# Performance work log

Measured on AMD Instinct MI355X. Metric: run time of the kernel, lower is better.

## Reference

```python
import jax, jax.numpy as jnp
import numpy as np

N_HEAD = 16


def setup_inputs() -> dict:
    key = jax.random.key(0)
    k1, k2, k3 = jax.random.split(key, 3)
    B, T, C = 4, 2048, 1024
    x = jax.random.normal(k1, (B, T, C), dtype=jnp.float32)
    W = jax.random.normal(k2, (3 * C, C), dtype=jnp.float32) * (1.0 / np.sqrt(C))
    b = jax.random.normal(k3, (3 * C,), dtype=jnp.float32) * 0.02
    return {"x": x, "W": W, "b": b, "input_pos": 0}


def reference(x, W, b, input_pos):
    # cache=False path; input_pos is unused (kept for signature fidelity).
    B, T, C = x.shape
    H = N_HEAD
    hs = C // H
    # Fused QKV projection: torch Linear is x @ W.T + b -> [B, T, 3C]
    qkv = (jnp.einsum('btc,oc->bto', x, W) + b).reshape(B, T, 3, H, hs)
    # q, k, v: [B, H, T, hs]
    q = jnp.transpose(qkv[:, :, 0], (0, 2, 1, 3))
    k = jnp.transpose(qkv[:, :, 1], (0, 2, 1, 3))
    v = jnp.transpose(qkv[:, :, 2], (0, 2, 1, 3))
    scale = hs ** (-0.5)
    # scores: [B, H, T, T]
    scores = jnp.einsum('bhqd,bhkd->bhqk', q, k) * scale
    causal = jnp.tril(jnp.ones((T, T), dtype=bool))
    scores = jnp.where(causal, scores, -jnp.inf)
    wei = jax.nn.softmax(scores, axis=-1)
    out = jnp.einsum('bhqk,bhkd->bhqd', wei, v)  # [B, H, T, hs]
    return jnp.transpose(out, (0, 2, 1, 3)).reshape(B, T, C)
```

## Files before the change

### kernel.cpp

```cpp
#include <hip/hip_runtime.h>
#include <stdint.h>

using s16x8 = __attribute__((ext_vector_type(8))) short;
using u16x8 = __attribute__((ext_vector_type(8))) unsigned short;
using f32x4 = __attribute__((ext_vector_type(4))) float;
using u32x2 = __attribute__((ext_vector_type(2))) uint32_t;

__device__ __forceinline__ unsigned short f2bf(float f) {
    union { float f; uint32_t u; } v; v.f = f;
    uint32_t u = (v.u + 0x7FFFu + ((v.u >> 16) & 1u)) >> 16;
    return (unsigned short)u;
}

#if defined(__has_builtin)
#if __has_builtin(__builtin_amdgcn_cvt_pk_bf16_f32)
#define HAS_PK_BF16 1
#endif
#endif

__device__ __forceinline__ uint32_t pk2bf(float x, float y) {
#ifdef HAS_PK_BF16
    typedef __bf16 bf16x2 __attribute__((ext_vector_type(2)));
    union { bf16x2 v; uint32_t u; } c;
    c.v = __builtin_amdgcn_cvt_pk_bf16_f32(x, y);
    return c.u;
#else
    union { float f; uint32_t u; } a, b; a.f = x; b.f = y;
    return ((a.u + 0x8000u) >> 16) | ((b.u + 0x8000u) & 0xffff0000u);
#endif
}

__device__ __forceinline__ f32x4 zero4() { f32x4 z = {0.f, 0.f, 0.f, 0.f}; return z; }

__device__ __forceinline__ void async16(const void* g, void* l) {
    __builtin_amdgcn_global_load_lds(
        reinterpret_cast<const uint32_t __attribute__((address_space(1)))*>(
            reinterpret_cast<uintptr_t>(g)),
        reinterpret_cast<uint32_t __attribute__((address_space(3)))*>(
            (uint32_t)reinterpret_cast<uintptr_t>(l)),
        16, 0, 0);
}

__global__ void cvt_bf16_2(const float* __restrict__ xa, unsigned short* __restrict__ oa, int na,
                           const float* __restrict__ xb, unsigned short* __restrict__ ob, int nb) {
    int i = (blockIdx.x * 256 + threadIdx.x) * 8;
    const float* in; unsigned short* out;
    if (i < na) { in = xa + i; out = oa + i; }
    else { int k = i - na; if (k >= nb) return; in = xb + k; out = ob + k; }
    f32x4 a = *(const f32x4*)(in);
    f32x4 c = *(const f32x4*)(in + 4);
    u16x8 o;
    o[0] = f2bf(a[0]); o[1] = f2bf(a[1]); o[2] = f2bf(a[2]); o[3] = f2bf(a[3]);
    o[4] = f2bf(c[0]); o[5] = f2bf(c[1]); o[6] = f2bf(c[2]); o[7] = f2bf(c[3]);
    *(u16x8*)(out) = o;
}

#define SC 0.18033688011112042f

__global__ __launch_bounds__(256, 2)
void qkv_gemm(const unsigned short* __restrict__ A,
              const unsigned short* __restrict__ Bw,
              const float* __restrict__ bias,
              unsigned short* __restrict__ Qo,
              unsigned short* __restrict__ Ko,
              unsigned short* __restrict__ Vto) {
    constexpr int Kd = 1024, T = 2048, H = 16;
    __shared__ __align__(16) unsigned short smem[128 * 136];
    unsigned short* const As = smem;
    unsigned short* const Bs = smem + 128 * 64;
    const int tid = threadIdx.x;
    const int wave = tid >> 6, lane = tid & 63;
    const int q4 = lane >> 4, l15 = lane & 15;
    const int bm = blockIdx.y * 128, bn = blockIdx.x * 128;
    const int wm = (wave >> 1) * 64, wn = (wave & 1) * 64;

    f32x4 acc[4][4];
#pragma unroll
    for (int a = 0; a < 4; ++a)
#pragma unroll
        for (int c = 0; c < 4; ++c) acc[a][c] = zero4();

    for (int k0 = 0; k0 < Kd; k0 += 64) {
#pragma unroll
        for (int r = 0; r < 4; ++r) {
            int u = r * 256 + tid;
            int row = u >> 3, su = (u & 7) ^ (row & 7);
            async16(A + (size_t)(bm + row) * Kd + k0 + su * 8, (char*)As + u * 16);
        }
#pragma unroll
        for (int r = 0; r < 4; ++r) {
            int u = r * 256 + tid;
            int row = u >> 3, su = (u & 7) ^ (row & 7);
            async16(Bw + (size_t)(bn + row) * Kd + k0 + su * 8, (char*)Bs + u * 16);
        }
        __syncthreads();
#pragma unroll
        for (int kt = 0; kt < 2; ++kt) {
            s16x8 af[4];
#pragma unroll
            for (int mt = 0; mt < 4; ++mt) {
                int row = wm + mt * 16 + l15;
                int uu = (kt * 4 + q4) ^ (row & 7);
                af[mt] = *(const s16x8*)(As + row * 64 + uu * 8);
            }
#pragma unroll
            for (int nt = 0; nt < 4; ++nt) {
                int row = wn + nt * 16 + l15;
                int uu = (kt * 4 + q4) ^ (row & 7);
                s16x8 bfv = *(const s16x8*)(Bs + row * 64 + uu * 8);
#pragma unroll
                for (int mt = 0; mt < 4; ++mt)
                    acc[mt][nt] = __builtin_amdgcn_mfma_f32_16x16x32_bf16(af[mt], bfv, acc[mt][nt], 0, 0, 0);
            }
        }
        __syncthreads();
    }
    if (bn >= 2048) {
#pragma unroll
        for (int nt = 0; nt < 4; ++nt) {
            int n = bn + wn + nt * 16 + l15;
            float bv = bias[n];
            int dl = wn + nt * 16 + l15;
#pragma unroll
            for (int mt = 0; mt < 4; ++mt)
#pragma unroll
                for (int i = 0; i < 4; ++i) {
                    int ml = wm + mt * 16 + 4 * q4 + i;
                    smem[dl * 136 + ml] = f2bf(acc[mt][nt][i] + bv);
                }
        }
        __syncthreads();
        const int bb = bm >> 11, t0 = bm & (T - 1);
#pragma unroll
        for (int rr = 0; rr < 8; ++rr) {
            int r = wave * 32 + rr * 4 + q4;
            int d = (bn - 2048) + r;
            int h = d >> 6, dd = d & 63;
            u16x8 v = *(const u16x8*)(smem + r * 136 + l15 * 8);
            *(u16x8*)(Vto + (((size_t)(bb * H + h)) * 64 + dd) * T + t0 + l15 * 8) = v;
        }
    } else {
#pragma unroll
        for (int nt = 0; nt < 4; ++nt) {
            int n = bn + wn + nt * 16 + l15;
            float bv = bias[n];
            int which = n >> 10, h = (n >> 6) & (H - 1), d = n & 63;
            unsigned short* dst = (which == 0) ? Qo : Ko;
            float scl = (which == 0) ? SC : 1.0f;
#pragma unroll
            for (int mt = 0; mt < 4; ++mt)
#pragma unroll
                for (int i = 0; i < 4; ++i) {
                    int m = bm + wm + mt * 16 + 4 * q4 + i;
                    int bb = m >> 11, t = m & (T - 1);
                    dst[((((size_t)bb * H + h) * T) + t) * 64 + d] = f2bf((acc[mt][nt][i] + bv) * scl);
                }
        }
    }
}

__global__ __launch_bounds__(256, 3)
void flash_attn(const unsigned short* __restrict__ Qg,
                const unsigned short* __restrict__ Kg,
                const unsigned short* __restrict__ Vtg,
                float* __restrict__ Out) {
    constexpr int T = 2048;
    __shared__ __align__(16) unsigned short Qs[128 * 64];
    __shared__ __align__(16) unsigned short Ks[2][64 * 64];
    __shared__ __align__(16) unsigned short Vt[2][64 * 64];

    const int tid = threadIdx.x;
    const int wave = tid >> 6, lane = tid & 63;
    const int q4 = lane >> 4, l15 = lane & 15;
    const int bh = blockIdx.x;
    const int qt = (int)gridDim.y - 1 - (int)blockIdx.y;
    const int b = bh >> 4, h = bh & 15;
    const int q0 = qt * 128;
    const unsigned short* qb = Qg + (size_t)bh * T * 64;
    const unsigned short* kb = Kg + (size_t)bh * T * 64;
    const unsigned short* vtb = Vtg + (size_t)bh * 64 * T;

#pragma unroll
    for (int r = 0; r < 4; ++r) {
        int u = r * 256 + tid;
        int row = u >> 3, su = (u & 7) ^ (row & 7);
        async16(qb + (size_t)(q0 + row) * 64 + su * 8, (char*)Qs + u * 16);
    }
#pragma unroll
    for (int r = 0; r < 2; ++r) {
        int u = r * 256 + tid;
        int row = u >> 3, su = (u & 7) ^ (row & 7);
        async16(kb + (size_t)row * 64 + su * 8, (char*)Ks[0] + u * 16);
        async16(vtb + (size_t)row * T + su * 8, (char*)Vt[0] + u * 16);
    }
    __syncthreads();
    s16x8 aq[2][2];
#pragma unroll
    for (int s = 0; s < 2; ++s)
#pragma unroll
        for (int kt = 0; kt < 2; ++kt) {
            int arow = s * 64 + wave * 16 + l15;
            int au = (kt * 4 + q4) ^ (arow & 7);
            aq[s][kt] = *(const s16x8*)(Qs + arow * 64 + au * 8);
        }
    __syncthreads();
    unsigned short* const Ps0 = Qs + (wave * 2 + 0) * 1024;
    unsigned short* const Ps1 = Qs + (wave * 2 + 1) * 1024;

    f32x4 oacc[2][4];
    float lsum[2] = {0.f, 0.f};
#pragma unroll
    for (int s = 0; s < 2; ++s)
#pragma unroll
        for (int ct = 0; ct < 4; ++ct) oacc[s][ct] = zero4();

    const int nkt = 2 * qt + 2;
    for (int j = 0; j < nkt; ++j) {
        if (j + 1 < nkt) {
            const int cn = (j + 1) * 64;
            unsigned short* kd = Ks[(j + 1) & 1];
            unsigned short* vd = Vt[(j + 1) & 1];
#pragma unroll
            for (int r = 0; r < 2; ++r) {
                int u = r * 256 + tid;
                int row = u >> 3, su = (u & 7) ^ (row & 7);
                async16(kb + (size_t)(cn + row) * 64 + su * 8, (char*)kd + u * 16);
                async16(vtb + (size_t)row * T + cn + su * 8, (char*)vd + u * 16);
            }
        }
        const unsigned short* kcur = Ks[j & 1];
        const unsigned short* vcur = Vt[j & 1];
        const int c0 = j * 64;
        const bool alive0 = (j <= 2 * qt);

        f32x4 sv[2][4];
#pragma unroll
        for (int s = 0; s < 2; ++s)
#pragma unroll
            for (int t = 0; t < 4; ++t) sv[s][t] = zero4();
#pragma unroll
        for (int kt = 0; kt < 2; ++kt) {
#pragma unroll
            for (int t = 0; t < 4; ++t) {
                int krow = t * 16 + l15;
                int ku = (kt * 4 + q4) ^ (krow & 7);
                s16x8 ak = *(const s16x8*)(kcur + krow * 64 + ku * 8);
                sv[0][t] = __builtin_amdgcn_mfma_f32_16x16x32_bf16(ak, aq[0][kt], sv[0][t], 0, 0, 0);
                sv[1][t] = __builtin_amdgcn_mfma_f32_16x16x32_bf16(ak, aq[1][kt], sv[1][t], 0, 0, 0);
            }
        }

#pragma unroll
        for (int s = 0; s < 2; ++s) {
            if (s == 0 && !alive0) continue;
            const bool dg = (j == 2 * qt + s);
            unsigned short* const ps = (s == 0) ? Ps0 : Ps1;
            const int qrow = q0 + s * 64 + wave * 16 + l15;
#pragma unroll
            for (int t = 0; t < 4; ++t) {
                float p0 = exp2f(sv[s][t][0]);
                float p1 = exp2f(sv[s][t][1]);
                float p2 = exp2f(sv[s][t][2]);
                float p3 = exp2f(sv[s][t][3]);
                if (dg) {
                    int col = c0 + t * 16 + 4 * q4;
                    if (col + 0 > qrow) p0 = 0.f;
                    if (col + 1 > qrow) p1 = 0.f;
                    if (col + 2 > qrow) p2 = 0.f;
                    if (col + 3 > qrow) p3 = 0.f;
                }
                lsum[s] += (p0 + p1) + (p2 + p3);
                u32x2 w;
                w[0] = pk2bf(p0, p1);
                w[1] = pk2bf(p2, p3);
                *(u32x2*)(ps + l15 * 64 + (((2 * t + (q4 >> 1)) ^ (l15 & 7)) << 3) +
                          ((q4 & 1) << 2)) = w;
            }
        }

#pragma unroll
        for (int kt = 0; kt < 2; ++kt) {
            int pu = ((kt * 4 + q4) ^ (l15 & 7)) * 8;
            s16x8 pa0, pa1;
            if (alive0) pa0 = *(const s16x8*)(Ps0 + l15 * 64 + pu);
            pa1 = *(const s16x8*)(Ps1 + l15 * 64 + pu);
#pragma unroll
            for (int ct = 0; ct < 4; ++ct) {
                int vrow = ct * 16 + l15;
                int vu = (kt * 4 + q4) ^ (vrow & 7);
                s16x8 vv = *(const s16x8*)(vcur + vrow * 64 + vu * 8);
                if (alive0)
                    oacc[0][ct] = __builtin_amdgcn_mfma_f32_16x16x32_bf16(pa0, vv, oacc[0][ct], 0, 0, 0);
                oacc[1][ct] = __builtin_amdgcn_mfma_f32_16x16x32_bf16(pa1, vv, oacc[1][ct], 0, 0, 0);
            }
        }
        __syncthreads();
    }
#pragma unroll
    for (int s = 0; s < 2; ++s) {
        float rs = lsum[s];
        rs += __shfl_xor(rs, 16, 64);
        rs += __shfl_xor(rs, 32, 64);
        float inv[4];
#pragma unroll
        for (int i = 0; i < 4; ++i)
            inv[i] = 1.0f / __shfl(rs, 4 * q4 + i, 64);
#pragma unroll
        for (int ct = 0; ct < 4; ++ct)
#pragma unroll
            for (int i = 0; i < 4; ++i) {
                int row = q0 + s * 64 + wave * 16 + 4 * q4 + i;
                Out[((size_t)b * T + row) * 1024 + h * 64 + ct * 16 + l15] =
                    oacc[s][ct][i] * inv[i];
            }
    }
}

extern "C" void kernel_launch(void* const* d_in, const int* in_sizes, int n_in,
                              void* d_out, int out_size, void* d_ws, size_t ws_size,
                              hipStream_t stream) {
    const float* x = (const float*)d_in[0];
    const float* W = (const float*)d_in[1];
    const float* bias = (const float*)d_in[2];
    float* out = (float*)d_out;

    unsigned short* xb = (unsigned short*)d_ws;
    unsigned short* wb = xb + 8388608;
    unsigned short* qb = wb + 3145728;
    unsigned short* kb = qb + 8388608;
    unsigned short* vtb = kb + 8388608;

    cvt_bf16_2<<<dim3((8388608 + 3145728) / 2048), dim3(256), 0, stream>>>(
        x, xb, 8388608, W, wb, 3145728);
    qkv_gemm<<<dim3(24, 64), dim3(256), 0, stream>>>(xb, wb, bias, qb, kb, vtb);
    flash_attn<<<dim3(64, 16), dim3(256), 0, stream>>>(qb, kb, vtb, out);
}
```

Before: 200.2 us.

## Replace double-buffered K/V prefetch with single-buffer sync load and fast exp2

Drops the double-buffered K/V LDS pipeline. Each iteration now loads the current K and V tile into a single buffer and then does a block barrier, which halves K/V shared memory and may allow more resident blocks. It also swaps exp2f for the hardware exp2 builtin to cut softmax instruction count. The cost is that load latency is no longer hidden behind compute, so each tile stalls on its own fetch.

```diff
diff --git a/kernel.cpp b/kernel.cpp
--- a/kernel.cpp
+++ b/kernel.cpp
@@ -16,7 +16,18 @@
 #if __has_builtin(__builtin_amdgcn_cvt_pk_bf16_f32)
 #define HAS_PK_BF16 1
 #endif
-#endif
+#if __has_builtin(__builtin_amdgcn_exp2f)
+#define HAS_EXP2 1
+#endif
+#endif
+
+__device__ __forceinline__ float fexp2(float x) {
+#ifdef HAS_EXP2
+    return __builtin_amdgcn_exp2f(x);
+#else
+    return __exp2f(x);
+#endif
+}
 
 __device__ __forceinline__ uint32_t pk2bf(float x, float y) {
 #ifdef HAS_PK_BF16
@@ -166,8 +177,8 @@
                 float* __restrict__ Out) {
     constexpr int T = 2048;
     __shared__ __align__(16) unsigned short Qs[128 * 64];
-    __shared__ __align__(16) unsigned short Ks[2][64 * 64];
-    __shared__ __align__(16) unsigned short Vt[2][64 * 64];
+    __shared__ __align__(16) unsigned short Ks[64 * 64];
+    __shared__ __align__(16) unsigned short Vt[64 * 64];
 
     const int tid = threadIdx.x;
     const int wave = tid >> 6, lane = tid & 63;
@@ -186,13 +197,6 @@
         int row = u >> 3, su = (u & 7) ^ (row & 7);
         async16(qb + (size_t)(q0 + row) * 64 + su * 8, (char*)Qs + u * 16);
     }
-#pragma unroll
-    for (int r = 0; r < 2; ++r) {
-        int u = r * 256 + tid;
-        int row = u >> 3, su = (u & 7) ^ (row & 7);
-        async16(kb + (size_t)row * 64 + su * 8, (char*)Ks[0] + u * 16);
-        async16(vtb + (size_t)row * T + su * 8, (char*)Vt[0] + u * 16);
-    }
     __syncthreads();
     s16x8 aq[2][2];
 #pragma unroll
@@ -216,21 +220,16 @@
 
     const int nkt = 2 * qt + 2;
     for (int j = 0; j < nkt; ++j) {
-        if (j + 1 < nkt) {
-            const int cn = (j + 1) * 64;
-            unsigned short* kd = Ks[(j + 1) & 1];
-            unsigned short* vd = Vt[(j + 1) & 1];
-#pragma unroll
-            for (int r = 0; r < 2; ++r) {
-                int u = r * 256 + tid;
-                int row = u >> 3, su = (u & 7) ^ (row & 7);
-                async16(kb + (size_t)(cn + row) * 64 + su * 8, (char*)kd + u * 16);
-                async16(vtb + (size_t)row * T + cn + su * 8, (char*)vd + u * 16);
-            }
-        }
-        const unsigned short* kcur = Ks[j & 1];
-        const unsigned short* vcur = Vt[j & 1];
         const int c0 = j * 64;
+#pragma unroll
+        for (int r = 0; r < 2; ++r) {
+            int u = r * 256 + tid;
+            int row = u >> 3, su = (u & 7) ^ (row & 7);
+            async16(kb + (size_t)(c0 + row) * 64 + su * 8, (char*)Ks + u * 16);
+            async16(vtb + (size_t)row * T + c0 + su * 8, (char*)Vt + u * 16);
+        }
+        __syncthreads();
+
         const bool alive0 = (j <= 2 * qt);
 
         f32x4 sv[2][4];
@@ -244,7 +243,7 @@
             for (int t = 0; t < 4; ++t) {
                 int krow = t * 16 + l15;
                 int ku = (kt * 4 + q4) ^ (krow & 7);
-                s16x8 ak = *(const s16x8*)(kcur + krow * 64 + ku * 8);
+                s16x8 ak = *(const s16x8*)(Ks + krow * 64 + ku * 8);
                 sv[0][t] = __builtin_amdgcn_mfma_f32_16x16x32_bf16(ak, aq[0][kt], sv[0][t], 0, 0, 0);
                 sv[1][t] = __builtin_amdgcn_mfma_f32_16x16x32_bf16(ak, aq[1][kt], sv[1][t], 0, 0, 0);
             }
@@ -258,10 +257,10 @@
             const int qrow = q0 + s * 64 + wave * 16 + l15;
 #pragma unroll
             for (int t = 0; t < 4; ++t) {
-                float p0 = exp2f(sv[s][t][0]);
-                float p1 = exp2f(sv[s][t][1]);
-                float p2 = exp2f(sv[s][t][2]);
-                float p3 = exp2f(sv[s][t][3]);
+                float p0 = fexp2(sv[s][t][0]);
+                float p1 = fexp2(sv[s][t][1]);
+                float p2 = fexp2(sv[s][t][2]);
+                float p3 = fexp2(sv[s][t][3]);
                 if (dg) {
                     int col = c0 + t * 16 + 4 * q4;
                     if (col + 0 > qrow) p0 = 0.f;
@@ -288,7 +287,7 @@
             for (int ct = 0; ct < 4; ++ct) {
                 int vrow = ct * 16 + l15;
                 int vu = (kt * 4 + q4) ^ (vrow & 7);
-                s16x8 vv = *(const s16x8*)(vcur + vrow * 64 + vu * 8);
+                s16x8 vv = *(const s16x8*)(Vt + vrow * 64 + vu * 8);
                 if (alive0)
                     oacc[0][ct] = __builtin_amdgcn_mfma_f32_16x16x32_bf16(pa0, vv, oacc[0][ct], 0, 0, 0);
                 oacc[1][ct] = __builtin_amdgcn_mfma_f32_16x16x32_bf16(pa1, vv, oacc[1][ct], 0, 0, 0);
```

Result: slower. 207.7 us (+3.7%).
